# Performance work log

Measured on AMD Instinct MI355X. Metric: run time of the kernel, lower is better.

Reference implementation:

```python
import jax, jax.numpy as jnp
import numpy as np

K_PRE_NMS = 2000      # number of top-scoring candidates fed to NMS
IOU_THRESHOLD = 0.5
IMAGE_SIZE = 800.0


def decode_boxes(deltas, locations, stride):
    """Faithful fcos_apply_deltas_to_locations (incl. the all(-1) special case
    and the swapped-y-coordinate convention of the source)."""
    d = deltas * stride
    x, y = locations[:, 0], locations[:, 1]
    boxes = jnp.stack([x - d[:, 0], y - d[:, 1], x + d[:, 2], y + d[:, 3]], axis=1)
    all_bg = jnp.all(deltas == -1)
    degen = jnp.stack([x, y, x, y], axis=1)
    return jnp.where(all_bg, degen, boxes)


def nms_keep_mask(boxes_sorted, iou_threshold):
    """Sequential NMS on score-descending-sorted boxes. Reproduces the source's
    exact (quirky) IoU math: y1=boxes[:,3], y2=boxes[:,1], w/h via abs().
    Returns bool keep mask aligned with the sorted order."""
    K = boxes_sorted.shape[0]
    x1, y1 = boxes_sorted[:, 0], boxes_sorted[:, 3]
    x2, y2 = boxes_sorted[:, 2], boxes_sorted[:, 1]
    area = (x2 - x1) * (y2 - y1)
    idx = jnp.arange(K)

    def body(i, state):
        active, keep = state
        is_kept = active[i]
        keep = keep.at[i].set(is_kept)
        xx1 = jnp.maximum(x1[i], x1)
        yy1 = jnp.minimum(y1[i], y1)
        xx2 = jnp.minimum(x2[i], x2)
        yy2 = jnp.maximum(y2[i], y2)
        inter = jnp.abs(xx2 - xx1) * jnp.abs(yy2 - yy1)
        iou = inter / (area[i] + area - inter)
        suppress = is_kept & (iou > iou_threshold) & (idx > i)
        return active & ~suppress, keep

    active0 = jnp.ones((K,), dtype=bool)
    keep0 = jnp.zeros((K,), dtype=bool)
    _, keep = jax.lax.fori_loop(0, K, body, (active0, keep0))
    return keep


def setup_inputs() -> dict:
    key = jax.random.key(0)
    k1, k2, k3 = jax.random.split(key, 3)
    N, C = 1048576, 20
    deltas = jax.random.normal(k1, (N, 4), dtype=jnp.float32) * 4.0 + 8.0
    locations = jax.random.uniform(k2, (N, 2), dtype=jnp.float32) * IMAGE_SIZE
    logits = jax.random.normal(k3, (N, C), dtype=jnp.float32)
    return {"deltas": deltas, "locations": locations, "logits": logits, "stride": 8}


def reference(deltas, locations, logits, stride):
    # 1) box delta decode (all N locations)
    boxes = decode_boxes(deltas, locations, stride)
    # 2) per-location best class score / class id
    probs = jax.nn.sigmoid(logits)              # [N, C]
    cls_scores = jnp.max(probs, axis=1)         # [N]
    class_ids = jnp.argmax(probs, axis=1)       # [N]
    # 3) pre-NMS top-k
    top_scores, top_idx = jax.lax.top_k(cls_scores, K_PRE_NMS)
    cand_boxes = boxes[top_idx]                 # [K, 4]
    cand_cls = class_ids[top_idx]               # [K]
    # 4) class-offset trick (class_spec_nms)
    max_coord = jnp.max(cand_boxes)
    offsets = cand_cls.astype(cand_boxes.dtype) * (max_coord + 1.0)
    boxes_for_nms = cand_boxes + offsets[:, None]
    # 5) sort by score descending (top_k already sorted; argsort is faithful to nms())
    order = jnp.argsort(-top_scores)
    keep = nms_keep_mask(boxes_for_nms[order], IOU_THRESHOLD)
    return cand_boxes[order], top_scores[order], cand_cls[order], keep
```

## Files before the change

### kernel.cpp

```cpp
#include <hip/hip_runtime.h>
#include <stdint.h>
#include <math.h>

#pragma clang fp contract(off)

#define N_ROWS 1048576
#define N_CLS  20
#define K_TOP  2000
#define CAND_MAX 4096
#define H_COPIES 4

#define SC_CNT  0
#define SC_MAXK 1
#define SC_DONE 2

static constexpr size_t OFF_MKEY  = 0;
static constexpr size_t OFF_CLS   = OFF_MKEY + 4ull * N_ROWS;
static constexpr size_t OFF_HIST1 = OFF_CLS + (size_t)N_ROWS;
static constexpr size_t OFF_HIST2 = OFF_HIST1 + 4096;
static constexpr size_t OFF_SCAL  = OFF_HIST2 + 4096;
static constexpr size_t OFF_GRP   = OFF_SCAL + 64;
static constexpr size_t OFF_CAND  = OFF_GRP + 256;
static constexpr size_t OFF_MASK  = OFF_CAND + 8ull * CAND_MAX;
static constexpr int ZERO_DWORDS = H_COPIES * 256 * 2 + 16 + 64;

__device__ __forceinline__ uint32_t mono_key(float f) {
    uint32_t u = __float_as_uint(f);
    return u ^ ((u & 0x80000000u) ? 0xFFFFFFFFu : 0x80000000u);
}
__device__ __forceinline__ float mono_inv(uint32_t k) {
    uint32_t u = (k & 0x80000000u) ? (k ^ 0x80000000u) : ~k;
    return __uint_as_float(u);
}

__global__ __launch_bounds__(256) void k_score(const float* __restrict__ logits,
                                               uint32_t* __restrict__ mkey,
                                               uint8_t* __restrict__ cls,
                                               uint32_t* __restrict__ zreg) {
    __shared__ uint32_t stage[256 * 21];
    int t = threadIdx.x;
    if (t < 4) {
        int zi = blockIdx.x * 4 + t;
        if (zi < ZERO_DWORDS) zreg[zi] = 0;
    }
    int waddr[20];
#pragma unroll
    for (int q = 0; q < 5; ++q) {
#pragma unroll
        for (int e = 0; e < 4; ++e) {
            int w = (q * 256 + t) * 4 + e;
            int r = w / 20, c = w - r * 20;
            waddr[q * 4 + e] = r * 21 + c;
        }
    }
    size_t blockRowBase = (size_t)blockIdx.x * 1024;
    for (int g = 0; g < 4; ++g) {
        const float4* src = (const float4*)(logits + (blockRowBase + (size_t)g * 256) * N_CLS);
#pragma unroll
        for (int q = 0; q < 5; ++q) {
            float4 v = src[q * 256 + t];
            stage[waddr[q * 4 + 0]] = __float_as_uint(v.x);
            stage[waddr[q * 4 + 1]] = __float_as_uint(v.y);
            stage[waddr[q * 4 + 2]] = __float_as_uint(v.z);
            stage[waddr[q * 4 + 3]] = __float_as_uint(v.w);
        }
        __syncthreads();
        const uint32_t* row = &stage[t * 21];
        float m = __uint_as_float(row[0]); int ci = 0;
#pragma unroll
        for (int c = 1; c < 20; ++c) {
            float v = __uint_as_float(row[c]);
            if (v > m) { m = v; ci = c; }
        }
        size_t rowIdx = blockRowBase + (size_t)g * 256 + t;
        mkey[rowIdx] = mono_key(m);
        cls[rowIdx] = (uint8_t)ci;
        __syncthreads();
    }
}

__global__ __launch_bounds__(256) void k_hist1(const uint32_t* __restrict__ mkey,
                                               uint32_t* __restrict__ hist1) {
    __shared__ uint32_t h[256];
    int t = threadIdx.x;
    h[t] = 0;
    __syncthreads();
    const uint4* m4 = (const uint4*)mkey;
    size_t base = (size_t)blockIdx.x * 1024;
    for (int it = 0; it < 4; ++it) {
        uint4 v = m4[base + it * 256 + t];
        atomicAdd(&h[v.x >> 24], 1u);
        atomicAdd(&h[v.y >> 24], 1u);
        atomicAdd(&h[v.z >> 24], 1u);
        atomicAdd(&h[v.w >> 24], 1u);
    }
    __syncthreads();
    uint32_t hv = h[t];
    if (hv) atomicAdd(&hist1[(blockIdx.x & (H_COPIES - 1)) * 256 + t], hv);
}

__device__ __forceinline__ void find8(const uint32_t* __restrict__ hist1,
                                      uint32_t* sfx, uint32_t* pb0, uint32_t* pR1,
                                      uint32_t& b0, uint32_t& R1) {
    int t = threadIdx.x;
    uint32_t h = 0;
#pragma unroll
    for (int k = 0; k < H_COPIES; ++k) h += hist1[k * 256 + t];
    sfx[t] = h;
    __syncthreads();
    for (int off = 1; off < 256; off <<= 1) {
        uint32_t v = (t + off < 256) ? sfx[t + off] : 0;
        __syncthreads();
        sfx[t] += v;
        __syncthreads();
    }
    if (sfx[t] >= (uint32_t)K_TOP && (t == 255 || sfx[t + 1] < (uint32_t)K_TOP)) {
        *pb0 = (uint32_t)t;
        *pR1 = (uint32_t)K_TOP - (sfx[t] - h);
    }
    __syncthreads();
    b0 = *pb0; R1 = *pR1;
}

__global__ __launch_bounds__(256) void k_hist2(const uint32_t* __restrict__ mkey,
                                               const uint32_t* __restrict__ hist1,
                                               uint32_t* __restrict__ hist2) {
    __shared__ uint32_t sfx[256];
    __shared__ uint32_t h2[256];
    __shared__ uint32_t sb0, sR1;
    int t = threadIdx.x;
    h2[t] = 0;
    uint32_t b0, R1;
    find8(hist1, sfx, &sb0, &sR1, b0, R1);
    uint4 v = ((const uint4*)mkey)[(size_t)blockIdx.x * 256 + t];
    if ((v.x >> 24) == b0) atomicAdd(&h2[(v.x >> 16) & 0xFFu], 1u);
    if ((v.y >> 24) == b0) atomicAdd(&h2[(v.y >> 16) & 0xFFu], 1u);
    if ((v.z >> 24) == b0) atomicAdd(&h2[(v.z >> 16) & 0xFFu], 1u);
    if ((v.w >> 24) == b0) atomicAdd(&h2[(v.w >> 16) & 0xFFu], 1u);
    __syncthreads();
    uint32_t hv = h2[t];
    if (hv) atomicAdd(&hist2[(blockIdx.x & (H_COPIES - 1)) * 256 + t], hv);
}

__global__ __launch_bounds__(256) void k_compact(const uint32_t* __restrict__ mkey,
                                                 const uint32_t* __restrict__ hist1,
                                                 const uint32_t* __restrict__ hist2,
                                                 uint32_t* __restrict__ scal,
                                                 uint64_t* __restrict__ cand) {
    __shared__ uint32_t sfx[256];
    __shared__ uint32_t sb0, sR1, sT;
    __shared__ uint32_t cnt, gbase;
    __shared__ uint64_t stg[1024];
    int t = threadIdx.x;
    int lane = t & 63;
    if (t == 0) cnt = 0;
    uint32_t b0, R1;
    find8(hist1, sfx, &sb0, &sR1, b0, R1);
    uint32_t h = 0;
#pragma unroll
    for (int k = 0; k < H_COPIES; ++k) h += hist2[k * 256 + t];
    __syncthreads();
    sfx[t] = h;
    __syncthreads();
    for (int off = 1; off < 256; off <<= 1) {
        uint32_t v = (t + off < 256) ? sfx[t + off] : 0;
        __syncthreads();
        sfx[t] += v;
        __syncthreads();
    }
    if (sfx[t] >= R1 && (t == 255 || sfx[t + 1] < R1)) {
        uint32_t t16 = (b0 << 8) | (uint32_t)t;
        sT = (t16 > 0) ? (t16 - 1) : 0;
    }
    __syncthreads();
    uint32_t T = sT;
    const uint4* m4 = (const uint4*)mkey;
    size_t base = (size_t)blockIdx.x * 1024;
    for (int it = 0; it < 4; ++it) {
        uint32_t r0 = (uint32_t)((base + it * 256 + t) * 4);
        uint4 v = m4[base + it * 256 + t];
#pragma unroll
        for (int e = 0; e < 4; ++e) {
            uint32_t u = (e == 0) ? v.x : (e == 1) ? v.y : (e == 2) ? v.z : v.w;
            bool pass = (u >> 16) >= T;
            unsigned long long bal = __ballot(pass);
            if (bal) {
                uint32_t wbase = 0;
                if (lane == 0) wbase = atomicAdd(&cnt, (uint32_t)__popcll(bal));
                wbase = __shfl(wbase, 0);
                if (pass) {
                    uint32_t pos = wbase + (uint32_t)__popcll(bal & ((1ull << lane) - 1ull));
                    if (pos < 1024) stg[pos] = ((uint64_t)u << 32) | (r0 + e);
                }
            }
        }
    }
    __syncthreads();
    uint32_t n = cnt; if (n > 1024) n = 1024;
    if (t == 0 && n) gbase = atomicAdd(&scal[SC_CNT], n);
    __syncthreads();
    if (n) {
        uint32_t gb = gbase;
        for (uint32_t i = t; i < n; i += 256) {
            uint32_t pos = gb + i;
            if (pos < (uint32_t)CAND_MAX) cand[pos] = stg[i];
        }
    }
}

__global__ __launch_bounds__(256) void k_rank(const uint64_t* __restrict__ cand,
                                              uint32_t* __restrict__ scal,
                                              const float* __restrict__ deltas,
                                              const float* __restrict__ locs,
                                              const int* __restrict__ stridep,
                                              const uint8_t* __restrict__ cls,
                                              float* __restrict__ out) {
    __shared__ uint64_t keys[CAND_MAX];
    __shared__ float red[4];
    int t = threadIdx.x;
    uint32_t M = scal[SC_CNT];
    if (M > (uint32_t)CAND_MAX) M = CAND_MAX;

    for (uint32_t i = t; i < M; i += 256) {
        uint64_t cd = cand[i];
        uint32_t mk = (uint32_t)(cd >> 32);
        uint32_t row = (uint32_t)cd & (N_ROWS - 1);
        float m = mono_inv(mk);
        float ef = (float)exp(-(double)m);
        float s = 1.0f / (1.0f + ef);
        keys[i] = ((uint64_t)(~__float_as_uint(s)) << 32) | row;
    }
    __syncthreads();

    uint32_t c = blockIdx.x * 256 + t;
    uint32_t rank = 0;
    uint64_t my = 0;
    if (c < M) {
        my = keys[c];
        uint32_t j = 0;
        for (; j + 4 <= M; j += 4) {
            ulonglong2 a = *(const ulonglong2*)&keys[j];
            ulonglong2 b = *(const ulonglong2*)&keys[j + 2];
            rank += (a.x < my) + (a.y < my) + (b.x < my) + (b.y < my);
        }
        for (; j < M; ++j) rank += (keys[j] < my);
    }

    float mx = -3.4e38f;
    if (c < M && rank < (uint32_t)K_TOP) {
        uint32_t row = (uint32_t)my & (N_ROWS - 1);
        float s = __uint_as_float(~(uint32_t)(my >> 32));
        float stridef = (float)(*stridep);
        float4 dl = ((const float4*)deltas)[row];
        float2 lc = ((const float2*)locs)[row];
        float d0 = dl.x * stridef, d1 = dl.y * stridef, d2 = dl.z * stridef, d3 = dl.w * stridef;
        float b0 = lc.x - d0, b1 = lc.y - d1, b2 = lc.x + d2, b3 = lc.y + d3;
        float4 bx = { b0, b1, b2, b3 };
        *(float4*)&out[4 * rank] = bx;
        out[8000 + rank] = s;
        out[10000 + rank] = (float)cls[row];
        mx = fmaxf(fmaxf(b0, b1), fmaxf(b2, b3));
    }
    for (int o = 32; o > 0; o >>= 1) mx = fmaxf(mx, __shfl_down(mx, o));
    if ((t & 63) == 0) red[t >> 6] = mx;
    __syncthreads();
    if (t == 0) {
        float m2 = fmaxf(fmaxf(red[0], red[1]), fmaxf(red[2], red[3]));
        atomicMax((unsigned int*)&scal[SC_MAXK], mono_key(m2));
    }
}

__global__ __launch_bounds__(256) void k_maskscan(const float* __restrict__ out_ro,
                                                  uint32_t* __restrict__ scal,
                                                  uint64_t* __restrict__ mask,
                                                  unsigned long long* __restrict__ grp,
                                                  float* __restrict__ out) {
    __shared__ int lastdone;
    int t = threadIdx.x;
    int lane = t & 63;
    int i = blockIdx.x * 4 + (t >> 6);
    float off1 = mono_inv(scal[SC_MAXK]) + 1.0f;
    float4 boxi = *(const float4*)&out_ro[4 * i];
    float oi = out_ro[10000 + i] * off1;
    float x1i = boxi.x + oi, y2i = boxi.y + oi, x2i = boxi.z + oi, y1i = boxi.w + oi;
    float ai = (x2i - x1i) * (y2i - y1i);
    unsigned long long dummy = 0;
    for (int jb = 0; jb < 32; ++jb) {
        int j = jb * 64 + lane;
        bool sup = false;
        if (j < K_TOP && j > i) {
            float4 boxj = *(const float4*)&out_ro[4 * j];
            float oj = out_ro[10000 + j] * off1;
            float x1j = boxj.x + oj, y2j = boxj.y + oj, x2j = boxj.z + oj, y1j = boxj.w + oj;
            float aj = (x2j - x1j) * (y2j - y1j);
            float xx1 = fmaxf(x1i, x1j);
            float yy1 = fminf(y1i, y1j);
            float xx2 = fminf(x2i, x2j);
            float yy2 = fmaxf(y2i, y2j);
            float inter = fabsf(xx2 - xx1) * fabsf(yy2 - yy1);
            float iou = inter / ((ai + aj) - inter);
            sup = iou > 0.5f;
        }
        unsigned long long bits = __ballot(sup);
        if (lane == 0) {
            dummy += atomicExch(&mask[(size_t)i * 32 + jb], bits);
            if (bits) dummy += atomicOr(&grp[i >> 6], 1ull << (i & 63));
        }
    }
    asm volatile("" :: "v"(dummy));
    asm volatile("s_waitcnt vmcnt(0) lgkmcnt(0)" ::: "memory");
    __syncthreads();
    if (t == 0) {
        unsigned old = atomicAdd(&scal[SC_DONE], 1u);
        lastdone = (old == (unsigned)(gridDim.x - 1)) ? 1 : 0;
    }
    __syncthreads();
    if (!lastdone) return;

    if (t < 64) {
        int l = t;
        uint64_t g = (l < 32) ? atomicOr(&grp[l], 0ull) : 0ull;
        uint64_t active = ~0ull;
        if (__ballot(g != 0ull)) {
            for (int gg = 0; gg < 32; ++gg) {
                uint64_t nz = __shfl(g, gg);
                while (nz) {
                    int b = __ffsll((long long)nz) - 1;
                    nz &= nz - 1;
                    int ii = gg * 64 + b;
                    uint64_t aw = __shfl(active, gg);
                    bool kept = (aw >> b) & 1ull;
                    uint64_t m = (l < 32) ? atomicOr(&mask[(size_t)ii * 32 + l], 0ull) : 0ull;
                    if (kept) active &= ~m;
                }
            }
        }
        if (l < 32) {
            int limit = K_TOP - l * 64;
            int nvec = limit < 64 ? limit / 4 : 16;
            for (int v = 0; v < nvec; ++v) {
                float4 f;
                f.x = ((active >> (4 * v + 0)) & 1ull) ? 1.0f : 0.0f;
                f.y = ((active >> (4 * v + 1)) & 1ull) ? 1.0f : 0.0f;
                f.z = ((active >> (4 * v + 2)) & 1ull) ? 1.0f : 0.0f;
                f.w = ((active >> (4 * v + 3)) & 1ull) ? 1.0f : 0.0f;
                *(float4*)&out[12000 + l * 64 + 4 * v] = f;
            }
        }
    }
}

extern "C" void kernel_launch(void* const* d_in, const int* in_sizes, int n_in,
                              void* d_out, int out_size, void* d_ws, size_t ws_size,
                              hipStream_t stream) {
    const float* deltas = (const float*)d_in[0];
    const float* locs   = (const float*)d_in[1];
    const float* logits = (const float*)d_in[2];
    const int*   stridep = (const int*)d_in[3];
    float* out = (float*)d_out;
    char* ws = (char*)d_ws;

    uint32_t* mkey  = (uint32_t*)(ws + OFF_MKEY);
    uint8_t*  cls   = (uint8_t*)(ws + OFF_CLS);
    uint32_t* hist1 = (uint32_t*)(ws + OFF_HIST1);
    uint32_t* hist2 = (uint32_t*)(ws + OFF_HIST2);
    uint32_t* scal  = (uint32_t*)(ws + OFF_SCAL);
    unsigned long long* grp = (unsigned long long*)(ws + OFF_GRP);
    uint64_t* cand  = (uint64_t*)(ws + OFF_CAND);
    uint64_t* mask  = (uint64_t*)(ws + OFF_MASK);

    k_score<<<dim3(1024), dim3(256), 0, stream>>>(logits, mkey, cls, hist1);
    k_hist1<<<dim3(256), dim3(256), 0, stream>>>(mkey, hist1);
    k_hist2<<<dim3(1024), dim3(256), 0, stream>>>(mkey, hist1, hist2);
    k_compact<<<dim3(256), dim3(256), 0, stream>>>(mkey, hist1, hist2, scal, cand);
    k_rank<<<dim3(16), dim3(256), 0, stream>>>(cand, scal, deltas, locs, stridep, cls, out);
    k_maskscan<<<dim3(500), dim3(256), 0, stream>>>(out, scal, mask, grp, out);
}
```

Baseline: 106.9 us.

## Fuse candidate compaction and ranking into one kernel via last-block-done pattern

Merges k_compact and k_rank into a single kernel of 64 blocks of 1024 threads. Each block compacts its candidates, then an atomic done-counter picks the last block, which ranks all candidates in shared memory and writes the top-K outputs and max coordinate. This removes one kernel launch and the gap between the two kernels. In exchange, the O(M^2) ranking now runs in a single block instead of 16, and candidate writes go through atomics for cross-block visibility.

```diff
diff --git a/kernel.cpp b/kernel.cpp
--- a/kernel.cpp
+++ b/kernel.cpp
@@ -10,9 +10,10 @@
 #define CAND_MAX 4096
 #define H_COPIES 4
 
-#define SC_CNT  0
-#define SC_MAXK 1
-#define SC_DONE 2
+#define SC_CNT   0
+#define SC_MAXK  1
+#define SC_DONE  2
+#define SC_DONE2 3
 
 static constexpr size_t OFF_MKEY  = 0;
 static constexpr size_t OFF_CLS   = OFF_MKEY + 4ull * N_ROWS;
@@ -104,17 +105,19 @@
                                       uint32_t& b0, uint32_t& R1) {
     int t = threadIdx.x;
     uint32_t h = 0;
-#pragma unroll
-    for (int k = 0; k < H_COPIES; ++k) h += hist1[k * 256 + t];
-    sfx[t] = h;
+    if (t < 256) {
+#pragma unroll
+        for (int k = 0; k < H_COPIES; ++k) h += hist1[k * 256 + t];
+        sfx[t] = h;
+    }
     __syncthreads();
     for (int off = 1; off < 256; off <<= 1) {
-        uint32_t v = (t + off < 256) ? sfx[t + off] : 0;
-        __syncthreads();
-        sfx[t] += v;
-        __syncthreads();
-    }
-    if (sfx[t] >= (uint32_t)K_TOP && (t == 255 || sfx[t + 1] < (uint32_t)K_TOP)) {
+        uint32_t v = (t < 256 && t + off < 256) ? sfx[t + off] : 0;
+        __syncthreads();
+        if (t < 256) sfx[t] += v;
+        __syncthreads();
+    }
+    if (t < 256 && sfx[t] >= (uint32_t)K_TOP && (t == 255 || sfx[t + 1] < (uint32_t)K_TOP)) {
         *pb0 = (uint32_t)t;
         *pR1 = (uint32_t)K_TOP - (sfx[t] - h);
     }
@@ -142,43 +145,54 @@
     if (hv) atomicAdd(&hist2[(blockIdx.x & (H_COPIES - 1)) * 256 + t], hv);
 }
 
-__global__ __launch_bounds__(256) void k_compact(const uint32_t* __restrict__ mkey,
-                                                 const uint32_t* __restrict__ hist1,
-                                                 const uint32_t* __restrict__ hist2,
-                                                 uint32_t* __restrict__ scal,
-                                                 uint64_t* __restrict__ cand) {
+__global__ __launch_bounds__(1024) void k_comprank(const uint32_t* __restrict__ mkey,
+                                                   const uint32_t* __restrict__ hist1,
+                                                   const uint32_t* __restrict__ hist2,
+                                                   uint32_t* __restrict__ scal,
+                                                   unsigned long long* __restrict__ cand,
+                                                   const float* __restrict__ deltas,
+                                                   const float* __restrict__ locs,
+                                                   const int* __restrict__ stridep,
+                                                   const uint8_t* __restrict__ cls,
+                                                   float* __restrict__ out) {
     __shared__ uint32_t sfx[256];
     __shared__ uint32_t sb0, sR1, sT;
     __shared__ uint32_t cnt, gbase;
     __shared__ uint64_t stg[1024];
+    __shared__ uint64_t keys[CAND_MAX];
+    __shared__ float red[16];
+    __shared__ int lastdone;
     int t = threadIdx.x;
     int lane = t & 63;
     if (t == 0) cnt = 0;
     uint32_t b0, R1;
     find8(hist1, sfx, &sb0, &sR1, b0, R1);
     uint32_t h = 0;
-#pragma unroll
-    for (int k = 0; k < H_COPIES; ++k) h += hist2[k * 256 + t];
-    __syncthreads();
-    sfx[t] = h;
+    if (t < 256) {
+#pragma unroll
+        for (int k = 0; k < H_COPIES; ++k) h += hist2[k * 256 + t];
+        sfx[t] = h;
+    }
     __syncthreads();
     for (int off = 1; off < 256; off <<= 1) {
-        uint32_t v = (t + off < 256) ? sfx[t + off] : 0;
-        __syncthreads();
-        sfx[t] += v;
-        __syncthreads();
-    }
-    if (sfx[t] >= R1 && (t == 255 || sfx[t + 1] < R1)) {
+        uint32_t v = (t < 256 && t + off < 256) ? sfx[t + off] : 0;
+        __syncthreads();
+        if (t < 256) sfx[t] += v;
+        __syncthreads();
+    }
+    if (t < 256 && sfx[t] >= R1 && (t == 255 || sfx[t + 1] < R1)) {
         uint32_t t16 = (b0 << 8) | (uint32_t)t;
         sT = (t16 > 0) ? (t16 - 1) : 0;
     }
     __syncthreads();
     uint32_t T = sT;
+
     const uint4* m4 = (const uint4*)mkey;
-    size_t base = (size_t)blockIdx.x * 1024;
+    size_t base = (size_t)blockIdx.x * 4096;
     for (int it = 0; it < 4; ++it) {
-        uint32_t r0 = (uint32_t)((base + it * 256 + t) * 4);
-        uint4 v = m4[base + it * 256 + t];
+        size_t i4 = base + (size_t)it * 1024 + t;
+        uint32_t r0 = (uint32_t)(i4 * 4);
+        uint4 v = m4[i4];
 #pragma unroll
         for (int e = 0; e < 4; ++e) {
             uint32_t u = (e == 0) ? v.x : (e == 1) ? v.y : (e == 2) ? v.z : v.w;
@@ -199,30 +213,29 @@
     uint32_t n = cnt; if (n > 1024) n = 1024;
     if (t == 0 && n) gbase = atomicAdd(&scal[SC_CNT], n);
     __syncthreads();
+    unsigned long long dummy = 0;
     if (n) {
         uint32_t gb = gbase;
-        for (uint32_t i = t; i < n; i += 256) {
+        for (uint32_t i = t; i < n; i += 1024) {
             uint32_t pos = gb + i;
-            if (pos < (uint32_t)CAND_MAX) cand[pos] = stg[i];
-        }
-    }
-}
-
-__global__ __launch_bounds__(256) void k_rank(const uint64_t* __restrict__ cand,
-                                              uint32_t* __restrict__ scal,
-                                              const float* __restrict__ deltas,
-                                              const float* __restrict__ locs,
-                                              const int* __restrict__ stridep,
-                                              const uint8_t* __restrict__ cls,
-                                              float* __restrict__ out) {
-    __shared__ uint64_t keys[CAND_MAX];
-    __shared__ float red[4];
-    int t = threadIdx.x;
-    uint32_t M = scal[SC_CNT];
+            if (pos < (uint32_t)CAND_MAX)
+                dummy += atomicExch(&cand[pos], (unsigned long long)stg[i]);
+        }
+    }
+    asm volatile("" :: "v"(dummy));
+    asm volatile("s_waitcnt vmcnt(0) lgkmcnt(0)" ::: "memory");
+    __syncthreads();
+    if (t == 0) {
+        unsigned old = atomicAdd(&scal[SC_DONE2], 1u);
+        lastdone = (old == (unsigned)(gridDim.x - 1)) ? 1 : 0;
+    }
+    __syncthreads();
+    if (!lastdone) return;
+
+    uint32_t M = atomicAdd(&scal[SC_CNT], 0u);
     if (M > (uint32_t)CAND_MAX) M = CAND_MAX;
-
-    for (uint32_t i = t; i < M; i += 256) {
-        uint64_t cd = cand[i];
+    for (uint32_t i = t; i < M; i += 1024) {
+        unsigned long long cd = atomicOr(&cand[i], 0ull);
         uint32_t mk = (uint32_t)(cd >> 32);
         uint32_t row = (uint32_t)cd & (N_ROWS - 1);
         float m = mono_inv(mk);
@@ -231,12 +244,11 @@
         keys[i] = ((uint64_t)(~__float_as_uint(s)) << 32) | row;
     }
     __syncthreads();
-
-    uint32_t c = blockIdx.x * 256 + t;
-    uint32_t rank = 0;
-    uint64_t my = 0;
-    if (c < M) {
-        my = keys[c];
+    float mx = -3.4e38f;
+    float stridef = (float)(*stridep);
+    for (uint32_t c = t; c < M; c += 1024) {
+        uint64_t my = keys[c];
+        uint32_t rank = 0;
         uint32_t j = 0;
         for (; j + 4 <= M; j += 4) {
             ulonglong2 a = *(const ulonglong2*)&keys[j];
@@ -244,29 +256,27 @@
             rank += (a.x < my) + (a.y < my) + (b.x < my) + (b.y < my);
         }
         for (; j < M; ++j) rank += (keys[j] < my);
-    }
-
-    float mx = -3.4e38f;
-    if (c < M && rank < (uint32_t)K_TOP) {
-        uint32_t row = (uint32_t)my & (N_ROWS - 1);
-        float s = __uint_as_float(~(uint32_t)(my >> 32));
-        float stridef = (float)(*stridep);
-        float4 dl = ((const float4*)deltas)[row];
-        float2 lc = ((const float2*)locs)[row];
-        float d0 = dl.x * stridef, d1 = dl.y * stridef, d2 = dl.z * stridef, d3 = dl.w * stridef;
-        float b0 = lc.x - d0, b1 = lc.y - d1, b2 = lc.x + d2, b3 = lc.y + d3;
-        float4 bx = { b0, b1, b2, b3 };
-        *(float4*)&out[4 * rank] = bx;
-        out[8000 + rank] = s;
-        out[10000 + rank] = (float)cls[row];
-        mx = fmaxf(fmaxf(b0, b1), fmaxf(b2, b3));
+        if (rank < (uint32_t)K_TOP) {
+            uint32_t row = (uint32_t)my & (N_ROWS - 1);
+            float s = __uint_as_float(~(uint32_t)(my >> 32));
+            float4 dl = ((const float4*)deltas)[row];
+            float2 lc = ((const float2*)locs)[row];
+            float d0 = dl.x * stridef, d1 = dl.y * stridef, d2 = dl.z * stridef, d3 = dl.w * stridef;
+            float b0f = lc.x - d0, b1f = lc.y - d1, b2f = lc.x + d2, b3f = lc.y + d3;
+            float4 bx = { b0f, b1f, b2f, b3f };
+            *(float4*)&out[4 * rank] = bx;
+            out[8000 + rank] = s;
+            out[10000 + rank] = (float)cls[row];
+            mx = fmaxf(mx, fmaxf(fmaxf(b0f, b1f), fmaxf(b2f, b3f)));
+        }
     }
     for (int o = 32; o > 0; o >>= 1) mx = fmaxf(mx, __shfl_down(mx, o));
     if ((t & 63) == 0) red[t >> 6] = mx;
     __syncthreads();
     if (t == 0) {
-        float m2 = fmaxf(fmaxf(red[0], red[1]), fmaxf(red[2], red[3]));
-        atomicMax((unsigned int*)&scal[SC_MAXK], mono_key(m2));
+        float m2 = red[0];
+        for (int i = 1; i < 16; ++i) m2 = fmaxf(m2, red[i]);
+        scal[SC_MAXK] = mono_key(m2);
     }
 }
 
@@ -366,13 +376,13 @@
     uint32_t* hist2 = (uint32_t*)(ws + OFF_HIST2);
     uint32_t* scal  = (uint32_t*)(ws + OFF_SCAL);
     unsigned long long* grp = (unsigned long long*)(ws + OFF_GRP);
-    uint64_t* cand  = (uint64_t*)(ws + OFF_CAND);
+    unsigned long long* cand = (unsigned long long*)(ws + OFF_CAND);
     uint64_t* mask  = (uint64_t*)(ws + OFF_MASK);
 
     k_score<<<dim3(1024), dim3(256), 0, stream>>>(logits, mkey, cls, hist1);
     k_hist1<<<dim3(256), dim3(256), 0, stream>>>(mkey, hist1);
     k_hist2<<<dim3(1024), dim3(256), 0, stream>>>(mkey, hist1, hist2);
-    k_compact<<<dim3(256), dim3(256), 0, stream>>>(mkey, hist1, hist2, scal, cand);
-    k_rank<<<dim3(16), dim3(256), 0, stream>>>(cand, scal, deltas, locs, stridep, cls, out);
+    k_comprank<<<dim3(64), dim3(1024), 0, stream>>>(mkey, hist1, hist2, scal, cand,
+                                                    deltas, locs, stridep, cls, out);
     k_maskscan<<<dim3(500), dim3(256), 0, stream>>>(out, scal, mask, grp, out);
 }
```

Result: slower. 188.3 us (+76.2%).

## Fuse scoring, top-byte and second-byte histograms into one persistent kernel with grid barrier

Applied to the files above, without the earlier changes.

Merges k_score, k_hist1 and k_hist2 into one 512-block kernel. Each block keeps its rows' mkeys, builds a local top-byte histogram, passes a global atomic barrier, finds the threshold bucket and builds the second-byte histogram from its own rows. Zeroing is done through magic-flagged handshakes, and zin is reset at the end of k_maskscan. k_rank is also reworked to be wave-per-candidate across 64 blocks. This removes two launches and a full reread of mkey for hist1, but relies on all 512 blocks being co-resident for the spin barrier, which risks deadlock.

```diff
diff --git a/kernel.cpp b/kernel.cpp
--- a/kernel.cpp
+++ b/kernel.cpp
@@ -9,10 +9,14 @@
 #define K_TOP  2000
 #define CAND_MAX 4096
 #define H_COPIES 4
-
-#define SC_CNT  0
-#define SC_MAXK 1
-#define SC_DONE 2
+#define MAGIC 0x5AD0C0DEu
+#define NBLK_SCORE 512
+
+#define SC_CNT   0
+#define SC_MAXK  1
+#define SC_DONE  2
+#define SC_BAR   3
+#define SC_FLAG  4
 
 static constexpr size_t OFF_MKEY  = 0;
 static constexpr size_t OFF_CLS   = OFF_MKEY + 4ull * N_ROWS;
@@ -20,9 +24,9 @@
 static constexpr size_t OFF_HIST2 = OFF_HIST1 + 4096;
 static constexpr size_t OFF_SCAL  = OFF_HIST2 + 4096;
 static constexpr size_t OFF_GRP   = OFF_SCAL + 64;
-static constexpr size_t OFF_CAND  = OFF_GRP + 256;
+static constexpr size_t OFF_ZIN   = OFF_GRP + 256;
+static constexpr size_t OFF_CAND  = OFF_ZIN + 256;
 static constexpr size_t OFF_MASK  = OFF_CAND + 8ull * CAND_MAX;
-static constexpr int ZERO_DWORDS = H_COPIES * 256 * 2 + 16 + 64;
 
 __device__ __forceinline__ uint32_t mono_key(float f) {
     uint32_t u = __float_as_uint(f);
@@ -33,36 +37,42 @@
     return __uint_as_float(u);
 }
 
-__global__ __launch_bounds__(256) void k_score(const float* __restrict__ logits,
-                                               uint32_t* __restrict__ mkey,
-                                               uint8_t* __restrict__ cls,
-                                               uint32_t* __restrict__ zreg) {
+__global__ __launch_bounds__(256, 4) void k_score(const float* __restrict__ logits,
+                                                  uint32_t* __restrict__ mkey,
+                                                  uint8_t* __restrict__ cls,
+                                                  uint32_t* __restrict__ hist1,
+                                                  uint32_t* __restrict__ hist2,
+                                                  uint32_t* __restrict__ scal,
+                                                  uint32_t* __restrict__ zin) {
     __shared__ uint32_t stage[256 * 21];
-    int t = threadIdx.x;
-    if (t < 4) {
-        int zi = blockIdx.x * 4 + t;
-        if (zi < ZERO_DWORDS) zreg[zi] = 0;
-    }
-    int waddr[20];
-#pragma unroll
-    for (int q = 0; q < 5; ++q) {
-#pragma unroll
-        for (int e = 0; e < 4; ++e) {
-            int w = (q * 256 + t) * 4 + e;
-            int r = w / 20, c = w - r * 20;
-            waddr[q * 4 + e] = r * 21 + c;
-        }
-    }
-    size_t blockRowBase = (size_t)blockIdx.x * 1024;
-    for (int g = 0; g < 4; ++g) {
-        const float4* src = (const float4*)(logits + (blockRowBase + (size_t)g * 256) * N_CLS);
+    __shared__ uint32_t h1[256];
+    __shared__ uint32_t sfx[256];
+    __shared__ uint32_t sb0;
+    int t = threadIdx.x, b = blockIdx.x;
+
+    if (b < 8) {
+        uint32_t zd = atomicExch(&hist1[b * 256 + t], 0u);
+        if (b == 7 && t < 80) zd += atomicExch(&hist1[2048 + t], 0u);
+        asm volatile("" :: "v"(zd));
+        asm volatile("s_waitcnt vmcnt(0)" ::: "memory");
+        __syncthreads();
+        if (t == 0) atomicExch(&zin[b], MAGIC);
+    }
+
+    h1[t] = 0;
+    __syncthreads();
+    size_t rowbase0 = (size_t)b * 2048;
+    for (int g = 0; g < 8; ++g) {
+        const float4* src = (const float4*)(logits + (rowbase0 + (size_t)g * 256) * N_CLS);
 #pragma unroll
         for (int q = 0; q < 5; ++q) {
             float4 v = src[q * 256 + t];
-            stage[waddr[q * 4 + 0]] = __float_as_uint(v.x);
-            stage[waddr[q * 4 + 1]] = __float_as_uint(v.y);
-            stage[waddr[q * 4 + 2]] = __float_as_uint(v.z);
-            stage[waddr[q * 4 + 3]] = __float_as_uint(v.w);
+            int w0 = (q * 256 + t) * 4;
+#pragma unroll
+            for (int e = 0; e < 4; ++e) {
+                int w = w0 + e;
+                stage[w + ((w * 52429u) >> 20)] = __float_as_uint((&v.x)[e]);
+            }
         }
         __syncthreads();
         const uint32_t* row = &stage[t * 21];
@@ -72,31 +82,61 @@
             float v = __uint_as_float(row[c]);
             if (v > m) { m = v; ci = c; }
         }
-        size_t rowIdx = blockRowBase + (size_t)g * 256 + t;
-        mkey[rowIdx] = mono_key(m);
-        cls[rowIdx] = (uint8_t)ci;
-        __syncthreads();
-    }
-}
-
-__global__ __launch_bounds__(256) void k_hist1(const uint32_t* __restrict__ mkey,
-                                               uint32_t* __restrict__ hist1) {
-    __shared__ uint32_t h[256];
-    int t = threadIdx.x;
-    h[t] = 0;
-    __syncthreads();
-    const uint4* m4 = (const uint4*)mkey;
-    size_t base = (size_t)blockIdx.x * 1024;
-    for (int it = 0; it < 4; ++it) {
-        uint4 v = m4[base + it * 256 + t];
-        atomicAdd(&h[v.x >> 24], 1u);
-        atomicAdd(&h[v.y >> 24], 1u);
-        atomicAdd(&h[v.z >> 24], 1u);
-        atomicAdd(&h[v.w >> 24], 1u);
-    }
-    __syncthreads();
-    uint32_t hv = h[t];
-    if (hv) atomicAdd(&hist1[(blockIdx.x & (H_COPIES - 1)) * 256 + t], hv);
+        size_t ri = rowbase0 + (size_t)g * 256 + t;
+        uint32_t u = mono_key(m);
+        mkey[ri] = u;
+        cls[ri] = (uint8_t)ci;
+        atomicAdd(&h1[u >> 24], 1u);
+        __syncthreads();
+    }
+
+    for (;;) {
+        int ok = 1;
+        if (t < 8) ok = (atomicAdd(&zin[t], 0u) == MAGIC) ? 1 : 0;
+        if (__syncthreads_count(ok) == 256) break;
+        __builtin_amdgcn_s_sleep(16);
+    }
+
+    uint32_t hv = h1[t], dm = 0;
+    if (hv) dm = atomicAdd(&hist1[(b & 3) * 256 + t], hv);
+    asm volatile("" :: "v"(dm));
+    asm volatile("s_waitcnt vmcnt(0)" ::: "memory");
+    __syncthreads();
+    if (t == 0) {
+        uint32_t old = atomicAdd(&scal[SC_BAR], 1u);
+        if (old == (uint32_t)(NBLK_SCORE - 1)) atomicExch(&scal[SC_FLAG], MAGIC);
+    }
+    for (;;) {
+        int ok = 1;
+        if (t == 0) ok = (atomicAdd(&scal[SC_FLAG], 0u) == MAGIC) ? 1 : 0;
+        if (__syncthreads_count(ok) == 256) break;
+        __builtin_amdgcn_s_sleep(64);
+    }
+
+    uint32_t hh = 0;
+#pragma unroll
+    for (int k = 0; k < H_COPIES; ++k) hh += atomicAdd(&hist1[k * 256 + t], 0u);
+    sfx[t] = hh;
+    __syncthreads();
+    for (int off = 1; off < 256; off <<= 1) {
+        uint32_t v = (t + off < 256) ? sfx[t + off] : 0;
+        __syncthreads();
+        sfx[t] += v;
+        __syncthreads();
+    }
+    if (sfx[t] >= (uint32_t)K_TOP && (t == 255 || sfx[t + 1] < (uint32_t)K_TOP)) sb0 = (uint32_t)t;
+    __syncthreads();
+    uint32_t b0 = sb0;
+
+    h1[t] = 0;
+    __syncthreads();
+    for (int g = 0; g < 8; ++g) {
+        uint32_t u = mkey[rowbase0 + (size_t)g * 256 + t];
+        if ((u >> 24) == b0) atomicAdd(&h1[(u >> 16) & 0xFFu], 1u);
+    }
+    __syncthreads();
+    hv = h1[t];
+    if (hv) atomicAdd(&hist2[(b & 3) * 256 + t], hv);
 }
 
 __device__ __forceinline__ void find8(const uint32_t* __restrict__ hist1,
@@ -122,31 +162,11 @@
     b0 = *pb0; R1 = *pR1;
 }
 
-__global__ __launch_bounds__(256) void k_hist2(const uint32_t* __restrict__ mkey,
-                                               const uint32_t* __restrict__ hist1,
-                                               uint32_t* __restrict__ hist2) {
-    __shared__ uint32_t sfx[256];
-    __shared__ uint32_t h2[256];
-    __shared__ uint32_t sb0, sR1;
-    int t = threadIdx.x;
-    h2[t] = 0;
-    uint32_t b0, R1;
-    find8(hist1, sfx, &sb0, &sR1, b0, R1);
-    uint4 v = ((const uint4*)mkey)[(size_t)blockIdx.x * 256 + t];
-    if ((v.x >> 24) == b0) atomicAdd(&h2[(v.x >> 16) & 0xFFu], 1u);
-    if ((v.y >> 24) == b0) atomicAdd(&h2[(v.y >> 16) & 0xFFu], 1u);
-    if ((v.z >> 24) == b0) atomicAdd(&h2[(v.z >> 16) & 0xFFu], 1u);
-    if ((v.w >> 24) == b0) atomicAdd(&h2[(v.w >> 16) & 0xFFu], 1u);
-    __syncthreads();
-    uint32_t hv = h2[t];
-    if (hv) atomicAdd(&hist2[(blockIdx.x & (H_COPIES - 1)) * 256 + t], hv);
-}
-
 __global__ __launch_bounds__(256) void k_compact(const uint32_t* __restrict__ mkey,
                                                  const uint32_t* __restrict__ hist1,
                                                  const uint32_t* __restrict__ hist2,
                                                  uint32_t* __restrict__ scal,
-                                                 uint64_t* __restrict__ cand) {
+                                                 unsigned long long* __restrict__ cand) {
     __shared__ uint32_t sfx[256];
     __shared__ uint32_t sb0, sR1, sT;
     __shared__ uint32_t cnt, gbase;
@@ -208,7 +228,7 @@
     }
 }
 
-__global__ __launch_bounds__(256) void k_rank(const uint64_t* __restrict__ cand,
+__global__ __launch_bounds__(256) void k_rank(const unsigned long long* __restrict__ cand,
                                               uint32_t* __restrict__ scal,
                                               const float* __restrict__ deltas,
                                               const float* __restrict__ locs,
@@ -216,13 +236,11 @@
                                               const uint8_t* __restrict__ cls,
                                               float* __restrict__ out) {
     __shared__ uint64_t keys[CAND_MAX];
-    __shared__ float red[4];
     int t = threadIdx.x;
     uint32_t M = scal[SC_CNT];
     if (M > (uint32_t)CAND_MAX) M = CAND_MAX;
-
     for (uint32_t i = t; i < M; i += 256) {
-        uint64_t cd = cand[i];
+        unsigned long long cd = cand[i];
         uint32_t mk = (uint32_t)(cd >> 32);
         uint32_t row = (uint32_t)cd & (N_ROWS - 1);
         float m = mono_inv(mk);
@@ -231,49 +249,37 @@
         keys[i] = ((uint64_t)(~__float_as_uint(s)) << 32) | row;
     }
     __syncthreads();
-
-    uint32_t c = blockIdx.x * 256 + t;
-    uint32_t rank = 0;
-    uint64_t my = 0;
-    if (c < M) {
-        my = keys[c];
-        uint32_t j = 0;
-        for (; j + 4 <= M; j += 4) {
-            ulonglong2 a = *(const ulonglong2*)&keys[j];
-            ulonglong2 b = *(const ulonglong2*)&keys[j + 2];
-            rank += (a.x < my) + (a.y < my) + (b.x < my) + (b.y < my);
-        }
-        for (; j < M; ++j) rank += (keys[j] < my);
-    }
-
-    float mx = -3.4e38f;
-    if (c < M && rank < (uint32_t)K_TOP) {
-        uint32_t row = (uint32_t)my & (N_ROWS - 1);
-        float s = __uint_as_float(~(uint32_t)(my >> 32));
-        float stridef = (float)(*stridep);
-        float4 dl = ((const float4*)deltas)[row];
-        float2 lc = ((const float2*)locs)[row];
-        float d0 = dl.x * stridef, d1 = dl.y * stridef, d2 = dl.z * stridef, d3 = dl.w * stridef;
-        float b0 = lc.x - d0, b1 = lc.y - d1, b2 = lc.x + d2, b3 = lc.y + d3;
-        float4 bx = { b0, b1, b2, b3 };
-        *(float4*)&out[4 * rank] = bx;
-        out[8000 + rank] = s;
-        out[10000 + rank] = (float)cls[row];
-        mx = fmaxf(fmaxf(b0, b1), fmaxf(b2, b3));
-    }
-    for (int o = 32; o > 0; o >>= 1) mx = fmaxf(mx, __shfl_down(mx, o));
-    if ((t & 63) == 0) red[t >> 6] = mx;
-    __syncthreads();
-    if (t == 0) {
-        float m2 = fmaxf(fmaxf(red[0], red[1]), fmaxf(red[2], red[3]));
-        atomicMax((unsigned int*)&scal[SC_MAXK], mono_key(m2));
-    }
+    int wid = t >> 6, lane = t & 63;
+    float stridef = (float)(*stridep);
+    float wmx = -3.4e38f;
+    for (uint32_t c = (uint32_t)blockIdx.x * 4 + wid; c < M; c += 256) {
+        uint64_t myk = keys[c];
+        uint32_t r = 0;
+        for (uint32_t j = lane; j < M; j += 64) r += (keys[j] < myk) ? 1u : 0u;
+#pragma unroll
+        for (int o = 32; o > 0; o >>= 1) r += __shfl_down(r, o);
+        if (lane == 0 && r < (uint32_t)K_TOP) {
+            uint32_t row = (uint32_t)myk & (N_ROWS - 1);
+            float s = __uint_as_float(~(uint32_t)(myk >> 32));
+            float4 dl = ((const float4*)deltas)[row];
+            float2 lc = ((const float2*)locs)[row];
+            float d0 = dl.x * stridef, d1 = dl.y * stridef, d2 = dl.z * stridef, d3 = dl.w * stridef;
+            float b0f = lc.x - d0, b1f = lc.y - d1, b2f = lc.x + d2, b3f = lc.y + d3;
+            float4 bx = { b0f, b1f, b2f, b3f };
+            *(float4*)&out[4 * r] = bx;
+            out[8000 + r] = s;
+            out[10000 + r] = (float)cls[row];
+            wmx = fmaxf(wmx, fmaxf(fmaxf(b0f, b1f), fmaxf(b2f, b3f)));
+        }
+    }
+    if (lane == 0) atomicMax(&scal[SC_MAXK], mono_key(wmx));
 }
 
 __global__ __launch_bounds__(256) void k_maskscan(const float* __restrict__ out_ro,
                                                   uint32_t* __restrict__ scal,
                                                   uint64_t* __restrict__ mask,
                                                   unsigned long long* __restrict__ grp,
+                                                  uint32_t* __restrict__ zin,
                                                   float* __restrict__ out) {
     __shared__ int lastdone;
     int t = threadIdx.x;
@@ -348,6 +354,7 @@
             }
         }
     }
+    if (t < 8) atomicExch(&zin[t], 0u);
 }
 
 extern "C" void kernel_launch(void* const* d_in, const int* in_sizes, int n_in,
@@ -366,13 +373,12 @@
     uint32_t* hist2 = (uint32_t*)(ws + OFF_HIST2);
     uint32_t* scal  = (uint32_t*)(ws + OFF_SCAL);
     unsigned long long* grp = (unsigned long long*)(ws + OFF_GRP);
-    uint64_t* cand  = (uint64_t*)(ws + OFF_CAND);
+    uint32_t* zin   = (uint32_t*)(ws + OFF_ZIN);
+    unsigned long long* cand = (unsigned long long*)(ws + OFF_CAND);
     uint64_t* mask  = (uint64_t*)(ws + OFF_MASK);
 
-    k_score<<<dim3(1024), dim3(256), 0, stream>>>(logits, mkey, cls, hist1);
-    k_hist1<<<dim3(256), dim3(256), 0, stream>>>(mkey, hist1);
-    k_hist2<<<dim3(1024), dim3(256), 0, stream>>>(mkey, hist1, hist2);
+    k_score<<<dim3(NBLK_SCORE), dim3(256), 0, stream>>>(logits, mkey, cls, hist1, hist2, scal, zin);
     k_compact<<<dim3(256), dim3(256), 0, stream>>>(mkey, hist1, hist2, scal, cand);
-    k_rank<<<dim3(16), dim3(256), 0, stream>>>(cand, scal, deltas, locs, stridep, cls, out);
-    k_maskscan<<<dim3(500), dim3(256), 0, stream>>>(out, scal, mask, grp, out);
-}
+    k_rank<<<dim3(64), dim3(256), 0, stream>>>(cand, scal, deltas, locs, stridep, cls, out);
+    k_maskscan<<<dim3(500), dim3(256), 0, stream>>>(out, scal, mask, grp, zin, out);
+}
```

Result: faster. 97.90 us (-8.4%).
